# Performance work log

Hardware: AMD Instinct MI355X
Metric: run time of the kernel (lower is better)

## Reference

```python
import jax, jax.numpy as jnp
from jax import lax
import numpy as np

B, T = 128, 270
NS = 8            # non-spatial features per step
IH = IW = 64      # spatial precip map
H_LSTM = 256
POOL = 4


def setup_inputs() -> dict:
    key = jax.random.key(0)
    ks = jax.random.split(key, 16)
    r = lambda k, s, sc=0.05: (jax.random.normal(k, s, dtype=jnp.float32) * sc)
    return {
        "x": jax.random.normal(ks[0], (B, T, NS + IH * IW), dtype=jnp.float32),
        "conv1_w": r(ks[1], (2, 1, 3, 3), 0.3),
        "conv1_b": r(ks[2], (2,)),
        "conv2_w": r(ks[3], (4, 2, 3, 3), 0.3),
        "conv2_b": r(ks[4], (4,)),
        "fc_w": r(ks[5], (8, 36), 0.2),
        "fc_b": r(ks[6], (8,)),
        "w_ih": r(ks[7], (4 * H_LSTM, NS + 8), 0.2),
        "w_hh": r(ks[8], (4 * H_LSTM, H_LSTM), 0.06),
        "b_ih": r(ks[9], (4 * H_LSTM,)),
        "b_hh": r(ks[10], (4 * H_LSTM,)),
        "head_w": r(ks[11], (1, H_LSTM), 0.06),
        "head_b": r(ks[12], (1,)),
        "h0": jax.random.normal(ks[13], (B, H_LSTM), dtype=jnp.float32),
        "c0": jax.random.normal(ks[14], (B, H_LSTM), dtype=jnp.float32),
    }


def _conv(z, w, b):
    y = lax.conv_general_dilated(z, w, (1, 1), "VALID",
                                 dimension_numbers=("NCHW", "OIHW", "NCHW"))
    return y + b[None, :, None, None]


def _maxpool(z):
    return lax.reduce_window(z, -jnp.inf, lax.max,
                             (1, 1, POOL, POOL), (1, 1, POOL, POOL), "VALID")


def reference(x, conv1_w, conv1_b, conv2_w, conv2_b, fc_w, fc_b,
              w_ih, w_hh, b_ih, b_hh, head_w, head_b, h0, c0):
    bsz = x.shape[0]
    xs = jnp.swapaxes(x, 0, 1)  # [T, B, NS + IH*IW]

    def step(carry, xt):
        h, c = carry
        x_sp = xt[:, NS:].reshape(bsz, 1, IH, IW)   # spatial precip map
        x_ns = xt[:, :NS]                           # non-spatial features
        o = _maxpool(jax.nn.relu(_conv(x_sp, conv1_w, conv1_b)))
        o = _maxpool(jax.nn.relu(_conv(o, conv2_w, conv2_b)))
        o = o.reshape(bsz, -1) @ fc_w.T + fc_b      # [B, 8]
        inp = jnp.concatenate([x_ns, o], axis=1)    # [B, NS+8]
        gates = inp @ w_ih.T + b_ih + h @ w_hh.T + b_hh  # [B, 4H]
        i, f, g, og = jnp.split(gates, 4, axis=1)   # torch LSTMCell gate order
        c_new = jax.nn.sigmoid(f) * c + jax.nn.sigmoid(i) * jnp.tanh(g)
        h_new = jax.nn.sigmoid(og) * jnp.tanh(c_new)
        return (h_new, c_new), h_new

    _, hs = lax.scan(step, (h0, c0), xs)            # hs: [T, B, H]
    out = jnp.swapaxes(hs, 0, 1) @ head_w.T + head_b  # [B, T, 1]; dropout = eval mode
    return out
```

## Files before the change

kernel.cpp:

```cpp
#include <hip/hip_runtime.h>

#define B_ 128
#define T_ 270
#define XR 4104

typedef __attribute__((ext_vector_type(8))) short short8v;
typedef __attribute__((ext_vector_type(4))) float f32x4;

__device__ inline unsigned short f2bf(float f) {
  unsigned u = __builtin_bit_cast(unsigned, f);
  u += 0x7fffu + ((u >> 16) & 1u);
  return (unsigned short)(u >> 16);
}
__device__ inline float sigm(float x) { return 1.0f / (1.0f + __expf(-x)); }
__device__ inline float tanh_f(float x) {
  float t = __expf(-2.0f * fabsf(x));
  float r = (1.0f - t) / (1.0f + t);
  return copysignf(r, x);
}

__global__ __launch_bounds__(256) void cnn_kernel(
    const float* __restrict__ x,
    const float* __restrict__ c1w_, const float* __restrict__ c1b_,
    const float* __restrict__ c2w_, const float* __restrict__ c2b_,
    const float* __restrict__ fcw, const float* __restrict__ fcb,
    const float* __restrict__ hdb,
    float* __restrict__ feat, unsigned* __restrict__ ctr,
    float* __restrict__ out)
{
  __shared__ float img[64 * 68];
  __shared__ float p1[2 * 15 * 16];
  __shared__ float p2[36];
  __shared__ float wsm[96];
  const int tid = threadIdx.x;
  const int bt = blockIdx.x;
  const int b = bt & 127, t = bt >> 7;

  if (bt == 0 && tid < 128) ctr[tid] = 0;

  const float* src = x + ((long)b * T_ + t) * XR;

  if (tid < 18) wsm[tid] = c1w_[tid];
  else if (tid < 20) wsm[tid] = c1b_[tid - 18];
  else if (tid < 92) wsm[tid] = c2w_[tid - 20];
  else if (tid < 96) wsm[tid] = c2b_[tid - 92];

  {
    const float4* s4 = (const float4*)(src + 8);
#pragma unroll
    for (int i0 = 0; i0 < 4; i0++) {
      int i = tid + i0 * 256;
      float4 v = s4[i];
      int e = i * 4;
      *((float4*)&img[(e >> 6) * 68 + (e & 63)]) = v;
    }
  }
  __syncthreads();

  if (tid < 225) {
    int py = tid / 15, px = tid - (tid / 15) * 15;
    float w0[9], w1[9];
#pragma unroll
    for (int j = 0; j < 9; j++) { w0[j] = wsm[j]; w1[j] = wsm[9 + j]; }
    const float b0 = wsm[18], b1v = wsm[19];
    float m0 = -1e30f, m1 = -1e30f;
    for (int dy = 0; dy < 4; dy++) {
      for (int dx = 0; dx < 4; dx++) {
        const float* ip = &img[(py * 4 + dy) * 68 + px * 4 + dx];
        float s0 = b0, s1 = b1v;
#pragma unroll
        for (int ky = 0; ky < 3; ky++) {
#pragma unroll
          for (int kx = 0; kx < 3; kx++) {
            float v = ip[ky * 68 + kx];
            s0 = fmaf(v, w0[ky * 3 + kx], s0);
            s1 = fmaf(v, w1[ky * 3 + kx], s1);
          }
        }
        m0 = fmaxf(m0, s0); m1 = fmaxf(m1, s1);
      }
    }
    p1[py * 16 + px] = fmaxf(m0, 0.f);
    p1[240 + py * 16 + px] = fmaxf(m1, 0.f);
  }
  __syncthreads();

  if (tid < 36) {
    int ch = tid / 9, rem = tid - ch * 9;
    int py = rem / 3, px = rem - py * 3;
    float m = -1e30f;
    for (int dy = 0; dy < 4; dy++) {
      for (int dx = 0; dx < 4; dx++) {
        int y = py * 4 + dy, xx = px * 4 + dx;
        float s = wsm[92 + ch];
#pragma unroll
        for (int ic = 0; ic < 2; ic++)
#pragma unroll
          for (int ky = 0; ky < 3; ky++)
#pragma unroll
            for (int kx = 0; kx < 3; kx++)
              s = fmaf(p1[ic * 240 + (y + ky) * 16 + xx + kx],
                       wsm[20 + ((ch * 2 + ic) * 3 + ky) * 3 + kx], s);
        m = fmaxf(m, s);
      }
    }
    p2[tid] = fmaxf(m, 0.f);
  }
  __syncthreads();

  float* fr = feat + ((long)t * B_ + b) * 16;
  if (tid < 8) {
    float s = fcb[tid];
#pragma unroll
    for (int j = 0; j < 36; j++) s = fmaf(p2[j], fcw[tid * 36 + j], s);
    fr[8 + tid] = s;
  } else if (tid < 16) {
    fr[tid - 8] = src[tid - 8];
  } else if (tid == 16) {
    out[(long)b * T_ + t] = hdb[0];
  }
}

__global__ __launch_bounds__(256, 1) void lstm_kernel(
    const float* __restrict__ feat, const float* __restrict__ whh,
    const float* __restrict__ wih, const float* __restrict__ bih,
    const float* __restrict__ bhh, const float* __restrict__ h0,
    const float* __restrict__ c0, const float* __restrict__ hw,
    unsigned* hb0, unsigned* hb1, unsigned* ctr, float* __restrict__ out)
{
  const int tid = threadIdx.x;
  const int wv = tid >> 6, lane = tid & 63;
  const int gb = blockIdx.x >> 2;
  const int hbk = blockIdx.x & 3;
  const int R0 = gb * 16, D0 = hbk * 64;
  __shared__ float gates[16 * 256];
  __shared__ float bias[256];
  unsigned* cptr = ctr + gb * 16;

  {
    int tau = tid >> 6, dl = tid & 63;
    int gr = tau * 256 + D0 + dl;
    bias[tid] = bih[gr] + bhh[gr];
  }

  const int col15 = lane & 15, ko = (lane >> 4) * 8;
  short8v bf[4][9];
  for (int nt = 0; nt < 4; nt++) {
    int gr = wv * 256 + D0 + nt * 16 + col15;
    const float* wr = whh + gr * 256;
#pragma unroll
    for (int kf = 0; kf < 8; kf++) {
      const float4* wp = (const float4*)(wr + kf * 32 + ko);
      float4 a = wp[0], bq = wp[1];
      short8v v;
      v[0] = f2bf(a.x); v[1] = f2bf(a.y); v[2] = f2bf(a.z); v[3] = f2bf(a.w);
      v[4] = f2bf(bq.x); v[5] = f2bf(bq.y); v[6] = f2bf(bq.z); v[7] = f2bf(bq.w);
      bf[nt][kf] = v;
    }
    short8v v = {0, 0, 0, 0, 0, 0, 0, 0};
    if (ko < 16) {
      const float4* wp = (const float4*)(wih + gr * 16 + ko);
      float4 a = wp[0], bq = wp[1];
      v[0] = f2bf(a.x); v[1] = f2bf(a.y); v[2] = f2bf(a.z); v[3] = f2bf(a.w);
      v[4] = f2bf(bq.x); v[5] = f2bf(bq.y); v[6] = f2bf(bq.z); v[7] = f2bf(bq.w);
    }
    bf[nt][8] = v;
  }

  const int dl2 = (tid & 31) * 2, er = tid >> 5;
  float cst[2][2];
#pragma unroll
  for (int p = 0; p < 2; p++) {
    int r = er + 8 * p;
    cst[p][0] = c0[(R0 + r) * 256 + D0 + dl2];
    cst[p][1] = c0[(R0 + r) * 256 + D0 + dl2 + 1];
    unsigned lo = f2bf(h0[(R0 + r) * 256 + D0 + dl2]);
    unsigned hi = f2bf(h0[(R0 + r) * 256 + D0 + dl2 + 1]);
    __hip_atomic_store(hb0 + (R0 + r) * 128 + ((D0 + dl2) >> 1), lo | (hi << 16),
                       __ATOMIC_RELAXED, __HIP_MEMORY_SCOPE_AGENT);
  }

  unsigned* hbr = hb0;
  unsigned* hbw = hb1;
  unsigned target = 4;

  __syncthreads();
  if (tid == 0) {
    __hip_atomic_fetch_add(cptr, 1u, __ATOMIC_ACQ_REL, __HIP_MEMORY_SCOPE_AGENT);
    long guard = 0;
    while (__hip_atomic_load(cptr, __ATOMIC_ACQUIRE, __HIP_MEMORY_SCOPE_AGENT) < target &&
           ++guard < (1L << 22)) {}
  }
  __syncthreads();

  const int ar = lane & 15;

  for (int t = 0; t < T_; t++) {
    short8v af[9];
    const unsigned long long* hrow =
        (const unsigned long long*)(hbr + (R0 + ar) * 128);
#pragma unroll
    for (int kf = 0; kf < 8; kf++) {
      int kq = kf * 8 + (ko >> 2);
      union { unsigned long long q[2]; short8v s; } u;
      u.q[0] = __hip_atomic_load(hrow + kq, __ATOMIC_RELAXED, __HIP_MEMORY_SCOPE_AGENT);
      u.q[1] = __hip_atomic_load(hrow + kq + 1, __ATOMIC_RELAXED, __HIP_MEMORY_SCOPE_AGENT);
      af[kf] = u.s;
    }
    {
      short8v v = {0, 0, 0, 0, 0, 0, 0, 0};
      if (ko < 16) {
        const float4* fp = (const float4*)(feat + ((long)t * B_ + R0 + ar) * 16 + ko);
        float4 a = fp[0], bq = fp[1];
        v[0] = f2bf(a.x); v[1] = f2bf(a.y); v[2] = f2bf(a.z); v[3] = f2bf(a.w);
        v[4] = f2bf(bq.x); v[5] = f2bf(bq.y); v[6] = f2bf(bq.z); v[7] = f2bf(bq.w);
      }
      af[8] = v;
    }

    f32x4 acc[4];
#pragma unroll
    for (int nt = 0; nt < 4; nt++) acc[nt] = (f32x4){0.f, 0.f, 0.f, 0.f};
#pragma unroll
    for (int kf = 0; kf < 9; kf++)
#pragma unroll
      for (int nt = 0; nt < 4; nt++)
        acc[nt] = __builtin_amdgcn_mfma_f32_16x16x32_bf16(af[kf], bf[nt][kf], acc[nt], 0, 0, 0);

    const int rb = (lane >> 4) * 4;
#pragma unroll
    for (int nt = 0; nt < 4; nt++)
#pragma unroll
      for (int rr = 0; rr < 4; rr++)
        gates[(rb + rr) * 256 + wv * 64 + nt * 16 + col15] = acc[nt][rr];
    __syncthreads();

#pragma unroll
    for (int p = 0; p < 2; p++) {
      int r = er + 8 * p;
      float hn2[2];
#pragma unroll
      for (int j = 0; j < 2; j++) {
        int dl = dl2 + j;
        float ipre = gates[r * 256 + dl] + bias[dl];
        float fpre = gates[r * 256 + 64 + dl] + bias[64 + dl];
        float gpre = gates[r * 256 + 128 + dl] + bias[128 + dl];
        float opre = gates[r * 256 + 192 + dl] + bias[192 + dl];
        float cn = sigm(fpre) * cst[p][j] + sigm(ipre) * tanh_f(gpre);
        cst[p][j] = cn;
        hn2[j] = sigm(opre) * tanh_f(cn);
      }
      unsigned pk = (unsigned)f2bf(hn2[0]) | ((unsigned)f2bf(hn2[1]) << 16);
      __hip_atomic_store(hbw + (R0 + r) * 128 + ((D0 + dl2) >> 1), pk,
                         __ATOMIC_RELAXED, __HIP_MEMORY_SCOPE_AGENT);
      float s = hn2[0] * hw[D0 + dl2] + hn2[1] * hw[D0 + dl2 + 1];
#pragma unroll
      for (int off = 16; off >= 1; off >>= 1) s += __shfl_xor(s, off);
      if ((lane & 31) == 0) atomicAdd(&out[(long)(R0 + r) * T_ + t], s);
    }

    { unsigned* tmp = hbr; hbr = hbw; hbw = tmp; }
    target += 4;
    __syncthreads();
    if (tid == 0) {
      __hip_atomic_fetch_add(cptr, 1u, __ATOMIC_ACQ_REL, __HIP_MEMORY_SCOPE_AGENT);
      long guard = 0;
      while (__hip_atomic_load(cptr, __ATOMIC_ACQUIRE, __HIP_MEMORY_SCOPE_AGENT) < target &&
             ++guard < (1L << 22)) {}
    }
    __syncthreads();
  }
}

extern "C" void kernel_launch(void* const* d_in, const int* in_sizes, int n_in,
                              void* d_out, int out_size, void* d_ws, size_t ws_size,
                              hipStream_t stream) {
  const float* x   = (const float*)d_in[0];
  const float* c1w = (const float*)d_in[1];
  const float* c1b = (const float*)d_in[2];
  const float* c2w = (const float*)d_in[3];
  const float* c2b = (const float*)d_in[4];
  const float* fcw = (const float*)d_in[5];
  const float* fcb = (const float*)d_in[6];
  const float* wih = (const float*)d_in[7];
  const float* whh = (const float*)d_in[8];
  const float* bih = (const float*)d_in[9];
  const float* bhh = (const float*)d_in[10];
  const float* hw  = (const float*)d_in[11];
  const float* hdb = (const float*)d_in[12];
  const float* h0  = (const float*)d_in[13];
  const float* c0  = (const float*)d_in[14];
  float* out = (float*)d_out;

  char* ws = (char*)d_ws;
  const size_t FEAT_B = (size_t)T_ * B_ * 16 * 4;
  const size_t HBUF_B = (size_t)B_ * 128 * 4;
  if (ws_size < FEAT_B + 2 * HBUF_B + 512) return;
  float* feat   = (float*)ws;
  unsigned* hb0 = (unsigned*)(ws + FEAT_B);
  unsigned* hb1 = (unsigned*)(ws + FEAT_B + HBUF_B);
  unsigned* ctr = (unsigned*)(ws + FEAT_B + 2 * HBUF_B);

  cnn_kernel<<<dim3(B_ * T_), dim3(256), 0, stream>>>(
      x, c1w, c1b, c2w, c2b, fcw, fcb, hdb, feat, ctr, out);
  lstm_kernel<<<dim3(32), dim3(256), 0, stream>>>(
      feat, whh, wih, bih, bhh, h0, c0, hw, hb0, hb1, ctr, out);
}
```

Baseline: 1.411 ms.

## Replace per-step counter barrier with per-block flags and overlap own-slice MFMAs

Swaps the shared atomic counter barrier for per-block monotonic flags that each block publishes after writing its hidden slice. Each wave polls the four peer flags in its batch group. Before waiting, the block computes the input-feature and its own hidden-slice MFMA contributions from a local LDS copy, so part of the recurrent matmul overlaps the wait. It also moves biases and head weights into registers and changes the block-to-group mapping. In exchange the synchronisation logic becomes more intricate, with a possible buffer-reuse race if a block runs ahead.

```diff
diff --git a/kernel.cpp b/kernel.cpp
--- a/kernel.cpp
+++ b/kernel.cpp
@@ -25,7 +25,7 @@
     const float* __restrict__ c2w_, const float* __restrict__ c2b_,
     const float* __restrict__ fcw, const float* __restrict__ fcb,
     const float* __restrict__ hdb,
-    float* __restrict__ feat, unsigned* __restrict__ ctr,
+    float* __restrict__ feat, unsigned* __restrict__ flags,
     float* __restrict__ out)
 {
   __shared__ float img[64 * 68];
@@ -36,7 +36,7 @@
   const int bt = blockIdx.x;
   const int b = bt & 127, t = bt >> 7;
 
-  if (bt == 0 && tid < 128) ctr[tid] = 0;
+  if (bt == 0 && tid < 32) flags[tid * 16] = 0;
 
   const float* src = x + ((long)b * T_ + t) * XR;
 
@@ -126,22 +126,15 @@
     const float* __restrict__ wih, const float* __restrict__ bih,
     const float* __restrict__ bhh, const float* __restrict__ h0,
     const float* __restrict__ c0, const float* __restrict__ hw,
-    unsigned* hb0, unsigned* hb1, unsigned* ctr, float* __restrict__ out)
+    unsigned* hb0, unsigned* hb1, unsigned* flags, float* __restrict__ out)
 {
   const int tid = threadIdx.x;
   const int wv = tid >> 6, lane = tid & 63;
-  const int gb = blockIdx.x >> 2;
-  const int hbk = blockIdx.x & 3;
+  const int gb = blockIdx.x & 7;
+  const int hbk = blockIdx.x >> 3;
   const int R0 = gb * 16, D0 = hbk * 64;
   __shared__ float gates[16 * 256];
-  __shared__ float bias[256];
-  unsigned* cptr = ctr + gb * 16;
-
-  {
-    int tau = tid >> 6, dl = tid & 63;
-    int gr = tau * 256 + D0 + dl;
-    bias[tid] = bih[gr] + bhh[gr];
-  }
+  __shared__ unsigned short hsl[16 * 88];
 
   const int col15 = lane & 15, ko = (lane >> 4) * 8;
   short8v bf[4][9];
@@ -169,6 +162,14 @@
 
   const int dl2 = (tid & 31) * 2, er = tid >> 5;
   float cst[2][2];
+  float bsr[4][2], hwr[2];
+#pragma unroll
+  for (int g = 0; g < 4; g++) {
+    int grr = g * 256 + D0 + dl2;
+    bsr[g][0] = bih[grr] + bhh[grr];
+    bsr[g][1] = bih[grr + 1] + bhh[grr + 1];
+  }
+  hwr[0] = hw[D0 + dl2]; hwr[1] = hw[D0 + dl2 + 1];
 #pragma unroll
   for (int p = 0; p < 2; p++) {
     int r = er + 8 * p;
@@ -176,56 +177,72 @@
     cst[p][1] = c0[(R0 + r) * 256 + D0 + dl2 + 1];
     unsigned lo = f2bf(h0[(R0 + r) * 256 + D0 + dl2]);
     unsigned hi = f2bf(h0[(R0 + r) * 256 + D0 + dl2 + 1]);
-    __hip_atomic_store(hb0 + (R0 + r) * 128 + ((D0 + dl2) >> 1), lo | (hi << 16),
+    unsigned pk = lo | (hi << 16);
+    __hip_atomic_store(hb0 + (R0 + r) * 128 + ((D0 + dl2) >> 1), pk,
                        __ATOMIC_RELAXED, __HIP_MEMORY_SCOPE_AGENT);
-  }
+    *(unsigned*)&hsl[r * 88 + dl2] = pk;
+  }
+  __syncthreads();
+  unsigned* myflag = flags + (gb * 4 + hbk) * 16;
+  if (tid == 0)
+    __hip_atomic_store(myflag, 1u, __ATOMIC_RELEASE, __HIP_MEMORY_SCOPE_AGENT);
 
   unsigned* hbr = hb0;
   unsigned* hbw = hb1;
-  unsigned target = 4;
-
-  __syncthreads();
-  if (tid == 0) {
-    __hip_atomic_fetch_add(cptr, 1u, __ATOMIC_ACQ_REL, __HIP_MEMORY_SCOPE_AGENT);
-    long guard = 0;
-    while (__hip_atomic_load(cptr, __ATOMIC_ACQUIRE, __HIP_MEMORY_SCOPE_AGENT) < target &&
-           ++guard < (1L << 22)) {}
-  }
-  __syncthreads();
-
   const int ar = lane & 15;
+  const int kfOwn = 2 * hbk;
+  unsigned* pollp = flags + (gb * 4 + (lane & 3)) * 16;
 
   for (int t = 0; t < T_; t++) {
-    short8v af[9];
+    short8v af8 = {0, 0, 0, 0, 0, 0, 0, 0};
+    if (ko < 16) {
+      const float4* fp = (const float4*)(feat + ((long)t * B_ + R0 + ar) * 16 + ko);
+      float4 a = fp[0], bq = fp[1];
+      af8[0] = f2bf(a.x); af8[1] = f2bf(a.y); af8[2] = f2bf(a.z); af8[3] = f2bf(a.w);
+      af8[4] = f2bf(bq.x); af8[5] = f2bf(bq.y); af8[6] = f2bf(bq.z); af8[7] = f2bf(bq.w);
+    }
+    short8v afO0 = *(const short8v*)&hsl[ar * 88 + ko];
+    short8v afO1 = *(const short8v*)&hsl[ar * 88 + 32 + ko];
+
+    f32x4 acc[4];
+#pragma unroll
+    for (int nt = 0; nt < 4; nt++) acc[nt] = (f32x4){0.f, 0.f, 0.f, 0.f};
+#pragma unroll
+    for (int nt = 0; nt < 4; nt++)
+      acc[nt] = __builtin_amdgcn_mfma_f32_16x16x32_bf16(af8, bf[nt][8], acc[nt], 0, 0, 0);
+#pragma unroll
+    for (int nt = 0; nt < 4; nt++)
+      acc[nt] = __builtin_amdgcn_mfma_f32_16x16x32_bf16(afO0, bf[nt][kfOwn], acc[nt], 0, 0, 0);
+#pragma unroll
+    for (int nt = 0; nt < 4; nt++)
+      acc[nt] = __builtin_amdgcn_mfma_f32_16x16x32_bf16(afO1, bf[nt][kfOwn + 1], acc[nt], 0, 0, 0);
+
+    {
+      const unsigned need = (unsigned)(t + 1);
+      bool ok; long guard = 0;
+      do {
+        unsigned v = (lane < 4)
+            ? __hip_atomic_load(pollp, __ATOMIC_RELAXED, __HIP_MEMORY_SCOPE_AGENT)
+            : need;
+        ok = __all((int)(v >= need));
+        if (!ok) __builtin_amdgcn_s_sleep(1);
+      } while (!ok && ++guard < (1L << 20));
+      __builtin_amdgcn_fence(__ATOMIC_ACQUIRE, "agent");
+    }
+
     const unsigned long long* hrow =
         (const unsigned long long*)(hbr + (R0 + ar) * 128);
 #pragma unroll
-    for (int kf = 0; kf < 8; kf++) {
+    for (int i = 0; i < 6; i++) {
+      int kf = (i < kfOwn) ? i : i + 2;
       int kq = kf * 8 + (ko >> 2);
       union { unsigned long long q[2]; short8v s; } u;
       u.q[0] = __hip_atomic_load(hrow + kq, __ATOMIC_RELAXED, __HIP_MEMORY_SCOPE_AGENT);
       u.q[1] = __hip_atomic_load(hrow + kq + 1, __ATOMIC_RELAXED, __HIP_MEMORY_SCOPE_AGENT);
-      af[kf] = u.s;
-    }
-    {
-      short8v v = {0, 0, 0, 0, 0, 0, 0, 0};
-      if (ko < 16) {
-        const float4* fp = (const float4*)(feat + ((long)t * B_ + R0 + ar) * 16 + ko);
-        float4 a = fp[0], bq = fp[1];
-        v[0] = f2bf(a.x); v[1] = f2bf(a.y); v[2] = f2bf(a.z); v[3] = f2bf(a.w);
-        v[4] = f2bf(bq.x); v[5] = f2bf(bq.y); v[6] = f2bf(bq.z); v[7] = f2bf(bq.w);
-      }
-      af[8] = v;
-    }
-
-    f32x4 acc[4];
-#pragma unroll
-    for (int nt = 0; nt < 4; nt++) acc[nt] = (f32x4){0.f, 0.f, 0.f, 0.f};
-#pragma unroll
-    for (int kf = 0; kf < 9; kf++)
 #pragma unroll
       for (int nt = 0; nt < 4; nt++)
-        acc[nt] = __builtin_amdgcn_mfma_f32_16x16x32_bf16(af[kf], bf[nt][kf], acc[nt], 0, 0, 0);
+        acc[nt] = __builtin_amdgcn_mfma_f32_16x16x32_bf16(u.s, bf[nt][kf], acc[nt], 0, 0, 0);
+    }
 
     const int rb = (lane >> 4) * 4;
 #pragma unroll
@@ -239,36 +256,37 @@
     for (int p = 0; p < 2; p++) {
       int r = er + 8 * p;
       float hn2[2];
-#pragma unroll
-      for (int j = 0; j < 2; j++) {
-        int dl = dl2 + j;
-        float ipre = gates[r * 256 + dl] + bias[dl];
-        float fpre = gates[r * 256 + 64 + dl] + bias[64 + dl];
-        float gpre = gates[r * 256 + 128 + dl] + bias[128 + dl];
-        float opre = gates[r * 256 + 192 + dl] + bias[192 + dl];
-        float cn = sigm(fpre) * cst[p][j] + sigm(ipre) * tanh_f(gpre);
-        cst[p][j] = cn;
-        hn2[j] = sigm(opre) * tanh_f(cn);
+      float2 gi = *(const float2*)&gates[r * 256 + dl2];
+      float2 gf = *(const float2*)&gates[r * 256 + 64 + dl2];
+      float2 gg = *(const float2*)&gates[r * 256 + 128 + dl2];
+      float2 go = *(const float2*)&gates[r * 256 + 192 + dl2];
+      {
+        float cn = sigm(gf.x + bsr[1][0]) * cst[p][0] +
+                   sigm(gi.x + bsr[0][0]) * tanh_f(gg.x + bsr[2][0]);
+        cst[p][0] = cn;
+        hn2[0] = sigm(go.x + bsr[3][0]) * tanh_f(cn);
+      }
+      {
+        float cn = sigm(gf.y + bsr[1][1]) * cst[p][1] +
+                   sigm(gi.y + bsr[0][1]) * tanh_f(gg.y + bsr[2][1]);
+        cst[p][1] = cn;
+        hn2[1] = sigm(go.y + bsr[3][1]) * tanh_f(cn);
       }
       unsigned pk = (unsigned)f2bf(hn2[0]) | ((unsigned)f2bf(hn2[1]) << 16);
       __hip_atomic_store(hbw + (R0 + r) * 128 + ((D0 + dl2) >> 1), pk,
                          __ATOMIC_RELAXED, __HIP_MEMORY_SCOPE_AGENT);
-      float s = hn2[0] * hw[D0 + dl2] + hn2[1] * hw[D0 + dl2 + 1];
+      *(unsigned*)&hsl[r * 88 + dl2] = pk;
+      float s = hn2[0] * hwr[0] + hn2[1] * hwr[1];
 #pragma unroll
       for (int off = 16; off >= 1; off >>= 1) s += __shfl_xor(s, off);
       if ((lane & 31) == 0) atomicAdd(&out[(long)(R0 + r) * T_ + t], s);
     }
 
+    __syncthreads();
+    if (tid == 0)
+      __hip_atomic_store(myflag, (unsigned)(t + 2),
+                         __ATOMIC_RELEASE, __HIP_MEMORY_SCOPE_AGENT);
     { unsigned* tmp = hbr; hbr = hbw; hbw = tmp; }
-    target += 4;
-    __syncthreads();
-    if (tid == 0) {
-      __hip_atomic_fetch_add(cptr, 1u, __ATOMIC_ACQ_REL, __HIP_MEMORY_SCOPE_AGENT);
-      long guard = 0;
-      while (__hip_atomic_load(cptr, __ATOMIC_ACQUIRE, __HIP_MEMORY_SCOPE_AGENT) < target &&
-             ++guard < (1L << 22)) {}
-    }
-    __syncthreads();
   }
 }
 
@@ -295,14 +313,14 @@
   char* ws = (char*)d_ws;
   const size_t FEAT_B = (size_t)T_ * B_ * 16 * 4;
   const size_t HBUF_B = (size_t)B_ * 128 * 4;
-  if (ws_size < FEAT_B + 2 * HBUF_B + 512) return;
-  float* feat   = (float*)ws;
-  unsigned* hb0 = (unsigned*)(ws + FEAT_B);
-  unsigned* hb1 = (unsigned*)(ws + FEAT_B + HBUF_B);
-  unsigned* ctr = (unsigned*)(ws + FEAT_B + 2 * HBUF_B);
+  if (ws_size < FEAT_B + 2 * HBUF_B + 4096) return;
+  float* feat     = (float*)ws;
+  unsigned* hb0   = (unsigned*)(ws + FEAT_B);
+  unsigned* hb1   = (unsigned*)(ws + FEAT_B + HBUF_B);
+  unsigned* flags = (unsigned*)(ws + FEAT_B + 2 * HBUF_B);
 
   cnn_kernel<<<dim3(B_ * T_), dim3(256), 0, stream>>>(
-      x, c1w, c1b, c2w, c2b, fcw, fcb, hdb, feat, ctr, out);
+      x, c1w, c1b, c2w, c2b, fcw, fcb, hdb, feat, flags, out);
   lstm_kernel<<<dim3(32), dim3(256), 0, stream>>>(
-      feat, whh, wih, bih, bhh, h0, c0, hw, hb0, hb1, ctr, out);
-}
+      feat, whh, wih, bih, bhh, h0, c0, hw, hb0, hb1, flags, out);
+}
```

Result: slower. 2.571 ms (+82.1%).

## Keep whole hidden dimension per block to drop cross-block spin barriers

Applied to the files above, without the earlier changes.

Each LSTM block now owns 16 batch rows and all 256 hidden units, using 8 waves with 8 gate tiles each. The hidden state lives in swizzled LDS rather than global buffers, and the per-step global atomic barrier across 4 blocks is gone. Gate nonlinearities run directly on MFMA accumulators with no gates staging in shared memory. The head output is reduced in LDS and written once per step instead of via atomicAdd. The cost is only 8 active CUs and twice the register weight footprint per thread, which may hurt occupancy or spill.

```diff
diff --git a/kernel.cpp b/kernel.cpp
--- a/kernel.cpp
+++ b/kernel.cpp
@@ -3,6 +3,7 @@
 #define B_ 128
 #define T_ 270
 #define XR 4104
+#define H_ 256
 
 typedef __attribute__((ext_vector_type(8))) short short8v;
 typedef __attribute__((ext_vector_type(4))) float f32x4;
@@ -24,9 +25,7 @@
     const float* __restrict__ c1w_, const float* __restrict__ c1b_,
     const float* __restrict__ c2w_, const float* __restrict__ c2b_,
     const float* __restrict__ fcw, const float* __restrict__ fcb,
-    const float* __restrict__ hdb,
-    float* __restrict__ feat, unsigned* __restrict__ ctr,
-    float* __restrict__ out)
+    float* __restrict__ feat)
 {
   __shared__ float img[64 * 68];
   __shared__ float p1[2 * 15 * 16];
@@ -36,8 +35,6 @@
   const int bt = blockIdx.x;
   const int b = bt & 127, t = bt >> 7;
 
-  if (bt == 0 && tid < 128) ctr[tid] = 0;
-
   const float* src = x + ((long)b * T_ + t) * XR;
 
   if (tid < 18) wsm[tid] = c1w_[tid];
@@ -116,101 +113,89 @@
     fr[8 + tid] = s;
   } else if (tid < 16) {
     fr[tid - 8] = src[tid - 8];
-  } else if (tid == 16) {
-    out[(long)b * T_ + t] = hdb[0];
-  }
-}
-
-__global__ __launch_bounds__(256, 1) void lstm_kernel(
+  }
+}
+
+__global__ __launch_bounds__(512, 1) void lstm_kernel(
     const float* __restrict__ feat, const float* __restrict__ whh,
     const float* __restrict__ wih, const float* __restrict__ bih,
     const float* __restrict__ bhh, const float* __restrict__ h0,
     const float* __restrict__ c0, const float* __restrict__ hw,
-    unsigned* hb0, unsigned* hb1, unsigned* ctr, float* __restrict__ out)
+    const float* __restrict__ hdb, float* __restrict__ out)
 {
   const int tid = threadIdx.x;
-  const int wv = tid >> 6, lane = tid & 63;
-  const int gb = blockIdx.x >> 2;
-  const int hbk = blockIdx.x & 3;
-  const int R0 = gb * 16, D0 = hbk * 64;
-  __shared__ float gates[16 * 256];
-  __shared__ float bias[256];
-  unsigned* cptr = ctr + gb * 16;
-
-  {
-    int tau = tid >> 6, dl = tid & 63;
-    int gr = tau * 256 + D0 + dl;
-    bias[tid] = bih[gr] + bhh[gr];
-  }
-
-  const int col15 = lane & 15, ko = (lane >> 4) * 8;
-  short8v bf[4][9];
-  for (int nt = 0; nt < 4; nt++) {
-    int gr = wv * 256 + D0 + nt * 16 + col15;
-    const float* wr = whh + gr * 256;
-#pragma unroll
-    for (int kf = 0; kf < 8; kf++) {
-      const float4* wp = (const float4*)(wr + kf * 32 + ko);
-      float4 a = wp[0], bq = wp[1];
-      short8v v;
-      v[0] = f2bf(a.x); v[1] = f2bf(a.y); v[2] = f2bf(a.z); v[3] = f2bf(a.w);
-      v[4] = f2bf(bq.x); v[5] = f2bf(bq.y); v[6] = f2bf(bq.z); v[7] = f2bf(bq.w);
-      bf[nt][kf] = v;
-    }
-    short8v v = {0, 0, 0, 0, 0, 0, 0, 0};
-    if (ko < 16) {
-      const float4* wp = (const float4*)(wih + gr * 16 + ko);
-      float4 a = wp[0], bq = wp[1];
-      v[0] = f2bf(a.x); v[1] = f2bf(a.y); v[2] = f2bf(a.z); v[3] = f2bf(a.w);
-      v[4] = f2bf(bq.x); v[5] = f2bf(bq.y); v[6] = f2bf(bq.z); v[7] = f2bf(bq.w);
-    }
-    bf[nt][8] = v;
-  }
-
-  const int dl2 = (tid & 31) * 2, er = tid >> 5;
-  float cst[2][2];
-#pragma unroll
-  for (int p = 0; p < 2; p++) {
-    int r = er + 8 * p;
-    cst[p][0] = c0[(R0 + r) * 256 + D0 + dl2];
-    cst[p][1] = c0[(R0 + r) * 256 + D0 + dl2 + 1];
-    unsigned lo = f2bf(h0[(R0 + r) * 256 + D0 + dl2]);
-    unsigned hi = f2bf(h0[(R0 + r) * 256 + D0 + dl2 + 1]);
-    __hip_atomic_store(hb0 + (R0 + r) * 128 + ((D0 + dl2) >> 1), lo | (hi << 16),
-                       __ATOMIC_RELAXED, __HIP_MEMORY_SCOPE_AGENT);
-  }
-
-  unsigned* hbr = hb0;
-  unsigned* hbw = hb1;
-  unsigned target = 4;
-
-  __syncthreads();
-  if (tid == 0) {
-    __hip_atomic_fetch_add(cptr, 1u, __ATOMIC_ACQ_REL, __HIP_MEMORY_SCOPE_AGENT);
-    long guard = 0;
-    while (__hip_atomic_load(cptr, __ATOMIC_ACQUIRE, __HIP_MEMORY_SCOPE_AGENT) < target &&
-           ++guard < (1L << 22)) {}
-  }
-  __syncthreads();
-
-  const int ar = lane & 15;
-
+  const int w = tid >> 6, lane = tid & 63;
+  const int R0 = blockIdx.x * 16;
+  const int col15 = lane & 15;
+  const int ko8 = (lane >> 4) * 8;
+  const int rb = (lane >> 4) * 4;
+  const int Dw = w * 32;
+
+  __shared__ unsigned short hls[16 * 256];
+  __shared__ float headp[8][20];
+
+  short8v bf[8][9];
+#pragma unroll
+  for (int g = 0; g < 4; g++) {
+#pragma unroll
+    for (int q = 0; q < 2; q++) {
+      const int col = g * 256 + Dw + q * 16 + col15;
+      const float* wr = whh + col * 256;
+#pragma unroll
+      for (int kf = 0; kf < 8; kf++) {
+        const float4* wp = (const float4*)(wr + kf * 32 + ko8);
+        float4 a = wp[0], bq = wp[1];
+        short8v v;
+        v[0] = f2bf(a.x); v[1] = f2bf(a.y); v[2] = f2bf(a.z); v[3] = f2bf(a.w);
+        v[4] = f2bf(bq.x); v[5] = f2bf(bq.y); v[6] = f2bf(bq.z); v[7] = f2bf(bq.w);
+        bf[g * 2 + q][kf] = v;
+      }
+      short8v v = {0, 0, 0, 0, 0, 0, 0, 0};
+      if (ko8 < 16) {
+        const float4* wp = (const float4*)(wih + col * 16 + ko8);
+        float4 a = wp[0], bq = wp[1];
+        v[0] = f2bf(a.x); v[1] = f2bf(a.y); v[2] = f2bf(a.z); v[3] = f2bf(a.w);
+        v[4] = f2bf(bq.x); v[5] = f2bf(bq.y); v[6] = f2bf(bq.z); v[7] = f2bf(bq.w);
+      }
+      bf[g * 2 + q][8] = v;
+    }
+  }
+
+  float bsr[8];
+#pragma unroll
+  for (int g = 0; g < 4; g++)
+#pragma unroll
+    for (int q = 0; q < 2; q++) {
+      const int col = g * 256 + Dw + q * 16 + col15;
+      bsr[g * 2 + q] = bih[col] + bhh[col];
+    }
+  float hwr[2] = { hw[Dw + col15], hw[Dw + 16 + col15] };
+  const float hdb0 = hdb[0];
+
+  float cs[2][4];
+#pragma unroll
+  for (int q = 0; q < 2; q++)
+#pragma unroll
+    for (int rr = 0; rr < 4; rr++) {
+      const int row = rb + rr, dim = Dw + q * 16 + col15;
+      cs[q][rr] = c0[(R0 + row) * H_ + dim];
+      const int byte = (row * 512 + dim * 2) ^ ((row & 7) << 4);
+      *(unsigned short*)((char*)hls + byte) = f2bf(h0[(R0 + row) * H_ + dim]);
+    }
+  __syncthreads();
+
+  const int ar = col15;
   for (int t = 0; t < T_; t++) {
     short8v af[9];
-    const unsigned long long* hrow =
-        (const unsigned long long*)(hbr + (R0 + ar) * 128);
 #pragma unroll
     for (int kf = 0; kf < 8; kf++) {
-      int kq = kf * 8 + (ko >> 2);
-      union { unsigned long long q[2]; short8v s; } u;
-      u.q[0] = __hip_atomic_load(hrow + kq, __ATOMIC_RELAXED, __HIP_MEMORY_SCOPE_AGENT);
-      u.q[1] = __hip_atomic_load(hrow + kq + 1, __ATOMIC_RELAXED, __HIP_MEMORY_SCOPE_AGENT);
-      af[kf] = u.s;
+      const int byte = (ar * 512 + kf * 64 + ko8 * 2) ^ ((ar & 7) << 4);
+      af[kf] = *(const short8v*)((const char*)hls + byte);
     }
     {
       short8v v = {0, 0, 0, 0, 0, 0, 0, 0};
-      if (ko < 16) {
-        const float4* fp = (const float4*)(feat + ((long)t * B_ + R0 + ar) * 16 + ko);
+      if (ko8 < 16) {
+        const float4* fp = (const float4*)(feat + ((long)t * B_ + R0 + ar) * 16 + ko8);
         float4 a = fp[0], bq = fp[1];
         v[0] = f2bf(a.x); v[1] = f2bf(a.y); v[2] = f2bf(a.z); v[3] = f2bf(a.w);
         v[4] = f2bf(bq.x); v[5] = f2bf(bq.y); v[6] = f2bf(bq.z); v[7] = f2bf(bq.w);
@@ -218,57 +203,55 @@
       af[8] = v;
     }
 
-    f32x4 acc[4];
-#pragma unroll
-    for (int nt = 0; nt < 4; nt++) acc[nt] = (f32x4){0.f, 0.f, 0.f, 0.f};
+    if (w == 0 && lane < 16 && t > 0) {
+      float s = hdb0;
+#pragma unroll
+      for (int i = 0; i < 8; i++) s += headp[i][lane];
+      out[(long)(R0 + lane) * T_ + (t - 1)] = s;
+    }
+    __syncthreads();
+
+    f32x4 acc[8];
+#pragma unroll
+    for (int u = 0; u < 8; u++) acc[u] = (f32x4){0.f, 0.f, 0.f, 0.f};
 #pragma unroll
     for (int kf = 0; kf < 9; kf++)
 #pragma unroll
-      for (int nt = 0; nt < 4; nt++)
-        acc[nt] = __builtin_amdgcn_mfma_f32_16x16x32_bf16(af[kf], bf[nt][kf], acc[nt], 0, 0, 0);
-
-    const int rb = (lane >> 4) * 4;
-#pragma unroll
-    for (int nt = 0; nt < 4; nt++)
-#pragma unroll
-      for (int rr = 0; rr < 4; rr++)
-        gates[(rb + rr) * 256 + wv * 64 + nt * 16 + col15] = acc[nt][rr];
+      for (int u = 0; u < 8; u++)
+        acc[u] = __builtin_amdgcn_mfma_f32_16x16x32_bf16(af[kf], bf[u][kf], acc[u], 0, 0, 0);
+
+    float ps[4] = {0.f, 0.f, 0.f, 0.f};
+#pragma unroll
+    for (int q = 0; q < 2; q++)
+#pragma unroll
+      for (int rr = 0; rr < 4; rr++) {
+        float i_ = acc[0 + q][rr] + bsr[0 + q];
+        float f_ = acc[2 + q][rr] + bsr[2 + q];
+        float g_ = acc[4 + q][rr] + bsr[4 + q];
+        float o_ = acc[6 + q][rr] + bsr[6 + q];
+        float cn = sigm(f_) * cs[q][rr] + sigm(i_) * tanh_f(g_);
+        cs[q][rr] = cn;
+        float hn = sigm(o_) * tanh_f(cn);
+        const int row = rb + rr, dim = Dw + q * 16 + col15;
+        const int byte = (row * 512 + dim * 2) ^ ((row & 7) << 4);
+        *(unsigned short*)((char*)hls + byte) = f2bf(hn);
+        ps[rr] += hn * hwr[q];
+      }
+#pragma unroll
+    for (int off = 1; off <= 8; off <<= 1)
+#pragma unroll
+      for (int rr = 0; rr < 4; rr++) ps[rr] += __shfl_xor(ps[rr], off);
+    if (col15 == 0)
+#pragma unroll
+      for (int rr = 0; rr < 4; rr++) headp[w][rb + rr] = ps[rr];
     __syncthreads();
-
-#pragma unroll
-    for (int p = 0; p < 2; p++) {
-      int r = er + 8 * p;
-      float hn2[2];
-#pragma unroll
-      for (int j = 0; j < 2; j++) {
-        int dl = dl2 + j;
-        float ipre = gates[r * 256 + dl] + bias[dl];
-        float fpre = gates[r * 256 + 64 + dl] + bias[64 + dl];
-        float gpre = gates[r * 256 + 128 + dl] + bias[128 + dl];
-        float opre = gates[r * 256 + 192 + dl] + bias[192 + dl];
-        float cn = sigm(fpre) * cst[p][j] + sigm(ipre) * tanh_f(gpre);
-        cst[p][j] = cn;
-        hn2[j] = sigm(opre) * tanh_f(cn);
-      }
-      unsigned pk = (unsigned)f2bf(hn2[0]) | ((unsigned)f2bf(hn2[1]) << 16);
-      __hip_atomic_store(hbw + (R0 + r) * 128 + ((D0 + dl2) >> 1), pk,
-                         __ATOMIC_RELAXED, __HIP_MEMORY_SCOPE_AGENT);
-      float s = hn2[0] * hw[D0 + dl2] + hn2[1] * hw[D0 + dl2 + 1];
-#pragma unroll
-      for (int off = 16; off >= 1; off >>= 1) s += __shfl_xor(s, off);
-      if ((lane & 31) == 0) atomicAdd(&out[(long)(R0 + r) * T_ + t], s);
-    }
-
-    { unsigned* tmp = hbr; hbr = hbw; hbw = tmp; }
-    target += 4;
-    __syncthreads();
-    if (tid == 0) {
-      __hip_atomic_fetch_add(cptr, 1u, __ATOMIC_ACQ_REL, __HIP_MEMORY_SCOPE_AGENT);
-      long guard = 0;
-      while (__hip_atomic_load(cptr, __ATOMIC_ACQUIRE, __HIP_MEMORY_SCOPE_AGENT) < target &&
-             ++guard < (1L << 22)) {}
-    }
-    __syncthreads();
+  }
+
+  if (w == 0 && lane < 16) {
+    float s = hdb0;
+#pragma unroll
+    for (int i = 0; i < 8; i++) s += headp[i][lane];
+    out[(long)(R0 + lane) * T_ + (T_ - 1)] = s;
   }
 }
 
@@ -292,17 +275,10 @@
   const float* c0  = (const float*)d_in[14];
   float* out = (float*)d_out;
 
-  char* ws = (char*)d_ws;
-  const size_t FEAT_B = (size_t)T_ * B_ * 16 * 4;
-  const size_t HBUF_B = (size_t)B_ * 128 * 4;
-  if (ws_size < FEAT_B + 2 * HBUF_B + 512) return;
-  float* feat   = (float*)ws;
-  unsigned* hb0 = (unsigned*)(ws + FEAT_B);
-  unsigned* hb1 = (unsigned*)(ws + FEAT_B + HBUF_B);
-  unsigned* ctr = (unsigned*)(ws + FEAT_B + 2 * HBUF_B);
+  float* feat = (float*)d_ws;
 
   cnn_kernel<<<dim3(B_ * T_), dim3(256), 0, stream>>>(
-      x, c1w, c1b, c2w, c2b, fcw, fcb, hdb, feat, ctr, out);
-  lstm_kernel<<<dim3(32), dim3(256), 0, stream>>>(
-      feat, whh, wih, bih, bhh, h0, c0, hw, hb0, hb1, ctr, out);
-}
+      x, c1w, c1b, c2w, c2b, fcw, fcb, feat);
+  lstm_kernel<<<dim3(8), dim3(512), 0, stream>>>(
+      feat, whh, wih, bih, bhh, h0, c0, hw, hdb, out);
+}
```

After: 3.154 ms. 124% more time.
